# Optimization experiments

Measured on AMD Instinct MI355X. Metric: run time of the kernel, lower is better.

The kernel has to match this reference:

```python
import jax, jax.numpy as jnp
import numpy as np


def setup_inputs() -> dict:
    key = jax.random.key(0)
    k1, k2 = jax.random.split(key)
    BATCH, SLOTS = 64, 65536   # 64 ciphertexts, 2^16 CKKS slots each
    NUM_T = 16                 # number of BSGS diagonal transforms (shifts 2^0..2^15)
    x = jax.random.normal(k1, (BATCH, SLOTS), dtype=jnp.float32)
    diagonals = jax.random.normal(k2, (NUM_T, SLOTS), dtype=jnp.float32)
    return {"x": x, "diagonals": diagonals, "stride": 1, "reps": 1}


def reference(x, diagonals, stride, reps):
    """FHE BSGS conv-as-linear-transform: rotate / plaintext-multiply / accumulate.

    Mirrors LinearTransform.evaluate_transforms:
      for i: out += roll(x, -2**i * stride) * diagonals[i]
      (two rescales are scale-management no-ops numerically)
      final conv roll by slots // (2 * reps).
    """
    slots = x.shape[-1]
    num_t = diagonals.shape[0]
    # Vectorize the rotations: gather all shifted copies at once.
    # shift for transform i is -2**i * stride (roll left by 2**i*stride).
    shifts = (2 ** jnp.arange(num_t, dtype=jnp.int32)) * stride        # [T]
    base = jnp.arange(slots, dtype=jnp.int32)                          # [S]
    idx = (base[None, :] + shifts[:, None]) % slots                    # [T, S] roll(-s) gather
    rolled = x[:, idx]                                                 # [B, T, S]
    out = jnp.einsum('bts,ts->bs', rolled, diagonals)                  # accumulate products
    # final conv roll: roll(slots // (2*reps)) => shift right
    out = jnp.roll(out, slots // (2 * reps), axis=-1)
    return out
```

## Files before the change

### kernel.cpp

```cpp
#include <hip/hip_runtime.h>


#define SLOTS 65536
#define MASK  65535
#define NB    4

__device__ __forceinline__ float4 shfl4(const float4 v, int lsel) {
    return make_float4(__shfl(v.x, lsel, 64), __shfl(v.y, lsel, 64),
                       __shfl(v.z, lsel, 64), __shfl(v.w, lsel, 64));
}

__global__ __launch_bounds__(256) void bsgs_kernel(
    const float* __restrict__ x,
    const float* __restrict__ diag,
    float* __restrict__ out)
{
    const int bid  = blockIdx.x;
    const int y    = bid & 15;
    const int xidx = bid >> 4;
    const int j    = xidx * 1024 + threadIdx.x * 4;
    const int bg   = y * NB;
    const int lane = threadIdx.x & 63;

    float4 dreg[16];
#pragma unroll
    for (int t = 0; t < 16; ++t)
        dreg[t] = *(const float4*)(diag + t * SLOTS + j);

    float4 acc[NB];
#pragma unroll
    for (int b = 0; b < NB; ++b) acc[b] = make_float4(0.f, 0.f, 0.f, 0.f);

#pragma unroll
    for (int b = 0; b < NB; ++b) {
        const float* __restrict__ xr = x + (size_t)(bg + b) * SLOTS;

        const float4 vA = *(const float4*)(xr + j);
        const float4 vE = *(const float4*)(xr + ((j + 256) & MASK));
        float4 vd[7];
#pragma unroll
        for (int t = 9; t < 16; ++t)
            vd[t - 9] = *(const float4*)(xr + ((j + (1 << t)) & MASK));

        float4 w[6];
#pragma unroll
        for (int i = 0; i < 6; ++i) {
            const int k  = 1 << i;
            const int lp = lane + k;
            const int ls = lp & 63;
            const float4 a = shfl4(vA, ls);
            const float4 e = shfl4(vE, ls);
            const bool useA = lp < 64;
            w[i] = make_float4(useA ? a.x : e.x, useA ? a.y : e.y,
                               useA ? a.z : e.z, useA ? a.w : e.w);
        }

        acc[b].x += vA.y   * dreg[0].x + vA.z   * dreg[1].x;
        acc[b].y += vA.z   * dreg[0].y + vA.w   * dreg[1].y;
        acc[b].z += vA.w   * dreg[0].z + w[0].x * dreg[1].z;
        acc[b].w += w[0].x * dreg[0].w + w[0].y * dreg[1].w;

#pragma unroll
        for (int t = 2; t <= 7; ++t) {
            const float4 v = w[t - 2];
            acc[b].x += v.x * dreg[t].x; acc[b].y += v.y * dreg[t].y;
            acc[b].z += v.z * dreg[t].z; acc[b].w += v.w * dreg[t].w;
        }
        acc[b].x += vE.x * dreg[8].x; acc[b].y += vE.y * dreg[8].y;
        acc[b].z += vE.z * dreg[8].z; acc[b].w += vE.w * dreg[8].w;
#pragma unroll
        for (int t = 9; t < 16; ++t) {
            const float4 v = vd[t - 9];
            acc[b].x += v.x * dreg[t].x; acc[b].y += v.y * dreg[t].y;
            acc[b].z += v.z * dreg[t].z; acc[b].w += v.w * dreg[t].w;
        }
    }

#pragma unroll
    for (int b = 0; b < NB; ++b)
        *(float4*)(out + (size_t)(bg + b) * SLOTS + (j ^ 32768)) = acc[b];
}

extern "C" void kernel_launch(void* const* d_in, const int* in_sizes, int n_in,
                              void* d_out, int out_size, void* d_ws, size_t ws_size,
                              hipStream_t stream) {
    const float* x    = (const float*)d_in[0];
    const float* diag = (const float*)d_in[1];
    float* out        = (float*)d_out;

    bsgs_kernel<<<dim3(1024), dim3(256), 0, stream>>>(x, diag, out);
}
```

Measured before the change: 84.72 us.

## Stage diagonals in LDS per column tile and remap blocks to row groups

Each block now covers a 256-column tile across 8 rows, two rows per wave. The block loads the 16 diagonal slices for that tile once into shared memory with nontemporal loads, and each wave reads its registers from there. Outputs are written with nontemporal stores, and the grid doubles to 2048 blocks. The aim is less redundant global diagonal traffic and more parallelism, at the cost of a __syncthreads barrier and fewer rows per thread to amortize the diagonal loads over.

```diff
diff --git a/kernel.cpp b/kernel.cpp
--- a/kernel.cpp
+++ b/kernel.cpp
@@ -3,7 +3,10 @@
 
 #define SLOTS 65536
 #define MASK  65535
-#define NB    4
+#define CTILE 256
+#define RPT   2
+
+typedef float vfloat4 __attribute__((ext_vector_type(4)));
 
 __device__ __forceinline__ float4 shfl4(const float4 v, int lsel) {
     return make_float4(__shfl(v.x, lsel, 64), __shfl(v.y, lsel, 64),
@@ -15,25 +18,38 @@
     const float* __restrict__ diag,
     float* __restrict__ out)
 {
+    __shared__ float dlds[16 * CTILE];
     const int bid  = blockIdx.x;
-    const int y    = bid & 15;
-    const int xidx = bid >> 4;
-    const int j    = xidx * 1024 + threadIdx.x * 4;
-    const int bg   = y * NB;
-    const int lane = threadIdx.x & 63;
+    const int g    = bid & 7;
+    const int c    = (bid >> 3) * CTILE;
+    const int tid  = threadIdx.x;
+    const int wave = tid >> 6;
+    const int lane = tid & 63;
+    const int j    = c + lane * 4;
+    const int row0 = g * 8 + wave * RPT;
+
+#pragma unroll
+    for (int k = 0; k < 4; ++k) {
+        const int F = tid + 256 * k;
+        const int t = F >> 6, q = F & 63;
+        const vfloat4 v = __builtin_nontemporal_load(
+            (const vfloat4*)(diag + t * SLOTS + c + q * 4));
+        *(vfloat4*)(dlds + t * CTILE + q * 4) = v;
+    }
+    __syncthreads();
 
     float4 dreg[16];
 #pragma unroll
     for (int t = 0; t < 16; ++t)
-        dreg[t] = *(const float4*)(diag + t * SLOTS + j);
+        dreg[t] = *(const float4*)(dlds + t * CTILE + lane * 4);
 
-    float4 acc[NB];
+    float4 acc[RPT];
 #pragma unroll
-    for (int b = 0; b < NB; ++b) acc[b] = make_float4(0.f, 0.f, 0.f, 0.f);
+    for (int r = 0; r < RPT; ++r) acc[r] = make_float4(0.f, 0.f, 0.f, 0.f);
 
 #pragma unroll
-    for (int b = 0; b < NB; ++b) {
-        const float* __restrict__ xr = x + (size_t)(bg + b) * SLOTS;
+    for (int r = 0; r < RPT; ++r) {
+        const float* __restrict__ xr = x + (size_t)(row0 + r) * SLOTS;
 
         const float4 vA = *(const float4*)(xr + j);
         const float4 vE = *(const float4*)(xr + ((j + 256) & MASK));
@@ -55,30 +71,34 @@
                                useA ? a.z : e.z, useA ? a.w : e.w);
         }
 
-        acc[b].x += vA.y   * dreg[0].x + vA.z   * dreg[1].x;
-        acc[b].y += vA.z   * dreg[0].y + vA.w   * dreg[1].y;
-        acc[b].z += vA.w   * dreg[0].z + w[0].x * dreg[1].z;
-        acc[b].w += w[0].x * dreg[0].w + w[0].y * dreg[1].w;
+        acc[r].x += vA.y   * dreg[0].x + vA.z   * dreg[1].x;
+        acc[r].y += vA.z   * dreg[0].y + vA.w   * dreg[1].y;
+        acc[r].z += vA.w   * dreg[0].z + w[0].x * dreg[1].z;
+        acc[r].w += w[0].x * dreg[0].w + w[0].y * dreg[1].w;
 
 #pragma unroll
         for (int t = 2; t <= 7; ++t) {
             const float4 v = w[t - 2];
-            acc[b].x += v.x * dreg[t].x; acc[b].y += v.y * dreg[t].y;
-            acc[b].z += v.z * dreg[t].z; acc[b].w += v.w * dreg[t].w;
+            acc[r].x += v.x * dreg[t].x; acc[r].y += v.y * dreg[t].y;
+            acc[r].z += v.z * dreg[t].z; acc[r].w += v.w * dreg[t].w;
         }
-        acc[b].x += vE.x * dreg[8].x; acc[b].y += vE.y * dreg[8].y;
-        acc[b].z += vE.z * dreg[8].z; acc[b].w += vE.w * dreg[8].w;
+        acc[r].x += vE.x * dreg[8].x; acc[r].y += vE.y * dreg[8].y;
+        acc[r].z += vE.z * dreg[8].z; acc[r].w += vE.w * dreg[8].w;
 #pragma unroll
         for (int t = 9; t < 16; ++t) {
             const float4 v = vd[t - 9];
-            acc[b].x += v.x * dreg[t].x; acc[b].y += v.y * dreg[t].y;
-            acc[b].z += v.z * dreg[t].z; acc[b].w += v.w * dreg[t].w;
+            acc[r].x += v.x * dreg[t].x; acc[r].y += v.y * dreg[t].y;
+            acc[r].z += v.z * dreg[t].z; acc[r].w += v.w * dreg[t].w;
         }
     }
 
 #pragma unroll
-    for (int b = 0; b < NB; ++b)
-        *(float4*)(out + (size_t)(bg + b) * SLOTS + (j ^ 32768)) = acc[b];
+    for (int r = 0; r < RPT; ++r) {
+        vfloat4 o;
+        o.x = acc[r].x; o.y = acc[r].y; o.z = acc[r].z; o.w = acc[r].w;
+        __builtin_nontemporal_store(o,
+            (vfloat4*)(out + (size_t)(row0 + r) * SLOTS + (j ^ 32768)));
+    }
 }
 
 extern "C" void kernel_launch(void* const* d_in, const int* in_sizes, int n_in,
@@ -88,5 +108,5 @@
     const float* diag = (const float*)d_in[1];
     float* out        = (float*)d_out;
 
-    bsgs_kernel<<<dim3(1024), dim3(256), 0, stream>>>(x, diag, out);
+    bsgs_kernel<<<dim3(2048), dim3(256), 0, stream>>>(x, diag, out);
 }
```

Result: slower. 92.35 us (+9.0%).
